# Kernel optimization log

Measured on AMD Instinct MI355X. Metric: run time of the kernel, lower is better.

The kernel has to match this reference:

```python
import jax, jax.numpy as jnp
import numpy as np

B, S, D_IN, D_OUT = 8, 2048, 1024, 64


def setup_inputs() -> dict:
    key = jax.random.key(0)
    ks = jax.random.split(key, 8)
    seq = jax.random.normal(ks[0], (B, S, D_IN), dtype=jnp.float32)
    mask = jax.random.bernoulli(ks[1], 0.15, (B, S))  # True = masked out
    lim = 1.0 / np.sqrt(D_IN)
    Wq = jax.random.uniform(ks[2], (D_IN, D_OUT), jnp.float32, -lim, lim)
    bq = jax.random.uniform(ks[3], (D_OUT,), jnp.float32, -lim, lim)
    Wk = jax.random.uniform(ks[4], (D_IN, D_OUT), jnp.float32, -lim, lim)
    bk = jax.random.uniform(ks[5], (D_OUT,), jnp.float32, -lim, lim)
    Wv = jax.random.uniform(ks[6], (D_IN, D_OUT), jnp.float32, -lim, lim)
    bv = jax.random.uniform(ks[7], (D_OUT,), jnp.float32, -lim, lim)
    return {"seq": seq, "mask": mask, "Wq": Wq, "bq": bq, "Wk": Wk, "bk": bk, "Wv": Wv, "bv": bv}


def reference(seq, mask, Wq, bq, Wk, bk, Wv, bv):
    q = jnp.einsum('bsd,df->bsf', seq, Wq) + bq  # [B,S,D_OUT]
    k = jnp.einsum('bsd,df->bsf', seq, Wk) + bk
    v = jnp.einsum('bsd,df->bsf', seq, Wv) + bv
    # NOTE: original code scales by sqrt(query.shape[1]) == sqrt(S), not sqrt(d)
    scale = jnp.asarray(q.shape[1], q.dtype) ** 0.5
    scores = jnp.einsum('bqf,bkf->bqk', q, k) / scale  # [B,S,S]
    scores = jnp.where(mask[:, None, :], jnp.asarray(-1e9, scores.dtype), scores)
    attn = jax.nn.softmax(scores, axis=-1)
    context = jnp.einsum('bqk,bkf->bqf', attn, v)  # [B,S,D_OUT]
    return context
```

## Files before the change

### kernel.cpp

```cpp
#include <hip/hip_runtime.h>
#include <hip/hip_bf16.h>
#include <stdint.h>

#define NB 8
#define SS 2048
#define DIN 1024
#define DOUT 64
#define MTOT (NB*SS)
#define SCALE 0.02209708691207961f

typedef short  short8 __attribute__((ext_vector_type(8)));
typedef float  f32x4  __attribute__((ext_vector_type(4)));
typedef unsigned short us4 __attribute__((ext_vector_type(4)));

#define WT_OFF 0
#define FM_OFF 393216
#define Q_OFF  524288
#define K_OFF  (Q_OFF + MTOT*DOUT*2)
#define VT_OFF (K_OFF + MTOT*DOUT*2)

__device__ __forceinline__ short f2bf(float f) {
  __bf16 h = (__bf16)f;
  return __builtin_bit_cast(short, h);
}

__device__ __forceinline__ void gl_lds16(const void* g, void* l) {
  __builtin_amdgcn_global_load_lds(
      (const __attribute__((address_space(1))) uint32_t*)g,
      (__attribute__((address_space(3))) uint32_t*)l, 16, 0, 0);
}

__global__ void k_prep(const float* __restrict__ Wq, const float* __restrict__ Wk,
                       const float* __restrict__ Wv, const void* __restrict__ mraw,
                       __bf16* __restrict__ Wt, float* __restrict__ fm) {
  int bid = blockIdx.x, t = threadIdx.x;
  if (bid < 48) {
    __shared__ float tile[64][65];
    int m = bid >> 4;
    int k0 = (bid & 15) * 64;
    const float* W = (m == 0) ? Wq : (m == 1 ? Wk : Wv);
    float sc = (m == 0) ? SCALE : 1.0f;
    #pragma unroll
    for (int i = 0; i < 16; i++) {
      int idx = i*256 + t;
      tile[idx >> 6][idx & 63] = W[(size_t)(k0 + (idx >> 6))*DOUT + (idx & 63)] * sc;
    }
    __syncthreads();
    #pragma unroll
    for (int i = 0; i < 16; i++) {
      int idx = i*256 + t;
      int n = idx >> 6, kk = idx & 63;
      Wt[(size_t)(m*DOUT + n)*DIN + k0 + kk] = (__bf16)tile[kk][n];
    }
  } else {
    __shared__ int bad[2];
    if (t < 2) bad[t] = 0;
    __syncthreads();
    const uint32_t* w = (const uint32_t*)mraw;
    int b0 = 0, b1 = 0;
    for (int i = t; i < 4096; i += 256) {
      uint32_t v = w[i];
      b0 |= !(v == 0u || v == 1u);
      b1 |= !(v == 0u || v == 0x3F800000u);
    }
    if (b0) atomicOr(&bad[0], 1);
    if (b1) atomicOr(&bad[1], 1);
    __syncthreads();
    int u8mode = bad[0] && bad[1];
    const uint8_t* p8 = (const uint8_t*)mraw;
    int i = (bid - 48)*256 + t;
    int mv = u8mode ? (p8[i] != 0) : (w[i] != 0u);
    fm[i] = mv ? 0.0f : 1.0f;
  }
}

__global__ __launch_bounds__(256) void k_qkv(
    const float* __restrict__ seq, const __bf16* __restrict__ Wt,
    const float* __restrict__ bq, const float* __restrict__ bk,
    const float* __restrict__ bv,
    __bf16* __restrict__ Qo, __bf16* __restrict__ Ko, __bf16* __restrict__ Vto) {
  __shared__ uint8_t smem[81920];
  int t = threadIdx.x, w = t >> 6, lane = t & 63, lg = lane >> 4, ll = lane & 15;
  int m0 = blockIdx.x * 64;
  const uint8_t* seqB = (const uint8_t*)seq;
  const uint8_t* WtB  = (const uint8_t*)Wt;

  f32x4 acc[12];
  #pragma unroll
  for (int i = 0; i < 12; i++) acc[i] = f32x4{0.f,0.f,0.f,0.f};

  auto STAGE = [&](int c) {
    uint8_t* bufA = smem + (c & 1)*40960;
    uint8_t* bufB = bufA + 16384;
    #pragma unroll
    for (int j = 0; j < 4; j++) {
      int g = j*256 + w*64 + lane;
      int r = g >> 4, u1 = g & 15;
      int u = u1 ^ (((r & 7) << 1) | ((r >> 3) & 1));
      gl_lds16(seqB + (size_t)(m0 + r)*4096 + c*256 + u*16,
               bufA + (j*256 + w*64)*16);
    }
    #pragma unroll
    for (int j = 0; j < 6; j++) {
      int g = j*256 + w*64 + lane;
      int R = g >> 3, u1 = g & 7;
      int u = u1 ^ (R & 7);
      gl_lds16(WtB + (size_t)R*2048 + c*128 + u*16,
               bufB + (j*256 + w*64)*16);
    }
  };

  STAGE(0);
  __syncthreads();
  for (int c = 0; c < 16; c++) {
    if (c < 15) STAGE(c + 1);
    uint8_t* bufA = smem + (c & 1)*40960;
    uint8_t* bufB = bufA + 16384;
    int r = w*16 + ll;
    int sa = ((r & 7) << 1) | ((r >> 3) & 1);
    short8 ab[2];
    #pragma unroll
    for (int kk = 0; kk < 2; kk++) {
      f32x4 a0 = *(const f32x4*)(bufA + r*256 + (((kk*8 + lg*2    ) ^ sa)*16));
      f32x4 a1 = *(const f32x4*)(bufA + r*256 + (((kk*8 + lg*2 + 1) ^ sa)*16));
      #pragma unroll
      for (int j = 0; j < 4; j++) { ab[kk][j] = f2bf(a0[j]); ab[kk][4+j] = f2bf(a1[j]); }
    }
    #pragma unroll
    for (int kk = 0; kk < 2; kk++) {
      #pragma unroll
      for (int mm = 0; mm < 12; mm++) {
        int R = mm*16 + ll;
        short8 bb = *(const short8*)(bufB + R*128 + (((kk*4 + lg) ^ (R & 7))*16));
        acc[mm] = __builtin_amdgcn_mfma_f32_16x16x32_bf16(ab[kk], bb, acc[mm], 0, 0, 0);
      }
    }
    __syncthreads();
  }

  int orow = m0 + w*16 + lg*4;
  int bb_  = orow >> 11;
  int sloc = orow & 2047;
  #pragma unroll
  for (int mm = 0; mm < 12; mm++) {
    int mat = mm >> 2;
    int col = (mm & 3)*16 + ll;
    float bias = (mat == 0) ? bq[col]*SCALE : (mat == 1 ? bk[col] : bv[col]);
    if (mat == 0) {
      #pragma unroll
      for (int rr = 0; rr < 4; rr++)
        Qo[(size_t)(orow + rr)*DOUT + col] = (__bf16)(acc[mm][rr] + bias);
    } else if (mat == 1) {
      #pragma unroll
      for (int rr = 0; rr < 4; rr++)
        Ko[(size_t)(orow + rr)*DOUT + col] = (__bf16)(acc[mm][rr] + bias);
    } else {
      us4 pk;
      #pragma unroll
      for (int rr = 0; rr < 4; rr++) pk[rr] = (unsigned short)f2bf(acc[mm][rr] + bias);
      *(us4*)((uint8_t*)Vto + ((size_t)(bb_*DOUT + col)*SS + sloc)*2) = pk;
    }
  }
}

__global__ __launch_bounds__(256) void k_attn(
    const __bf16* __restrict__ Q, const __bf16* __restrict__ Kd,
    const __bf16* __restrict__ Vt, const float* __restrict__ fm,
    float* __restrict__ out) {
  __shared__ uint8_t smem[90112];
  float* fml = (float*)(smem + 81920);
  int t = threadIdx.x, w = t >> 6, lane = t & 63, lg = lane >> 4, ll = lane & 15;
  int b = blockIdx.x >> 5, qt = blockIdx.x & 31;
  int q0 = qt*64 + w*16;

  for (int i = t; i < SS; i += 256) fml[i] = fm[b*SS + i];

  const uint8_t* qbase = (const uint8_t*)Q + ((size_t)(b*SS + q0 + ll))*128;
  short8 aq[2];
  aq[0] = *(const short8*)(qbase + lg*16);
  aq[1] = *(const short8*)(qbase + 64 + lg*16);

  f32x4 oacc[4];
  #pragma unroll
  for (int i = 0; i < 4; i++) oacc[i] = f32x4{0.f,0.f,0.f,0.f};
  float den[4] = {0.f, 0.f, 0.f, 0.f};

  const uint8_t* kgb = (const uint8_t*)Kd + (size_t)b*SS*128;
  const uint8_t* vgb = (const uint8_t*)Vt + (size_t)b*DOUT*SS*2;
  uint8_t* pbase = smem + 65536 + w*4096;

  auto STAGE = [&](int kb, int bi) {
    uint8_t* bk_ = smem + bi*32768;
    uint8_t* bv_ = bk_ + 16384;
    #pragma unroll
    for (int j = 0; j < 4; j++) {
      int g = j*256 + w*64 + lane;
      int key = g >> 3, u1 = g & 7;
      int u = u1 ^ (key & 7);
      gl_lds16(kgb + (size_t)(kb*128 + key)*128 + u*16, bk_ + (j*256 + w*64)*16);
    }
    #pragma unroll
    for (int j = 0; j < 4; j++) {
      int g = j*256 + w*64 + lane;
      int d = g >> 4, u1 = g & 15;
      int u = u1 ^ (d & 15);
      gl_lds16(vgb + (size_t)d*4096 + kb*256 + u*16, bv_ + (j*256 + w*64)*16);
    }
  };

  STAGE(0, 0);
  __syncthreads();
  for (int kb = 0; kb < 16; kb++) {
    if (kb < 15) STAGE(kb + 1, (kb + 1) & 1);
    uint8_t* bk_ = smem + (kb & 1)*32768;
    uint8_t* bv_ = bk_ + 16384;
    f32x4 sacc[8];
    #pragma unroll
    for (int i = 0; i < 8; i++) sacc[i] = f32x4{0.f,0.f,0.f,0.f};
    #pragma unroll
    for (int kk = 0; kk < 2; kk++) {
      #pragma unroll
      for (int nf = 0; nf < 8; nf++) {
        int key = nf*16 + ll;
        short8 kf = *(const short8*)(bk_ + key*128 + (((kk*4 + lg) ^ (key & 7))*16));
        sacc[nf] = __builtin_amdgcn_mfma_f32_16x16x32_bf16(aq[kk], kf, sacc[nf], 0, 0, 0);
      }
    }
    #pragma unroll
    for (int nf = 0; nf < 8; nf++) {
      float msk = fml[kb*128 + nf*16 + ll];
      #pragma unroll
      for (int r = 0; r < 4; r++) {
        float p = msk * __expf(sacc[nf][r]);
        __bf16 pb = (__bf16)p;
        den[r] += (float)pb;
        int qrow = lg*4 + r;
        int col = nf*16 + ll;
        *(__bf16*)(pbase + qrow*256 + (((col >> 3) ^ qrow)*16) + (col & 7)*2) = pb;
      }
    }
    #pragma unroll
    for (int ks = 0; ks < 4; ks++) {
      int u = ks*4 + lg;
      short8 pf = *(const short8*)(pbase + ll*256 + ((u ^ ll)*16));
      #pragma unroll
      for (int df = 0; df < 4; df++) {
        int d = df*16 + ll;
        short8 vf = *(const short8*)(bv_ + d*256 + ((u ^ (d & 15))*16));
        oacc[df] = __builtin_amdgcn_mfma_f32_16x16x32_bf16(pf, vf, oacc[df], 0, 0, 0);
      }
    }
    __syncthreads();
  }
  #pragma unroll
  for (int r = 0; r < 4; r++) {
    float d = den[r];
    d += __shfl_xor(d, 1, 64);
    d += __shfl_xor(d, 2, 64);
    d += __shfl_xor(d, 4, 64);
    d += __shfl_xor(d, 8, 64);
    den[r] = d;
  }
  #pragma unroll
  for (int df = 0; df < 4; df++) {
    int col = df*16 + ll;
    #pragma unroll
    for (int r = 0; r < 4; r++) {
      int gq = b*SS + q0 + lg*4 + r;
      out[(size_t)gq*DOUT + col] = oacc[df][r] / den[r];
    }
  }
}

extern "C" void kernel_launch(void* const* d_in, const int* in_sizes, int n_in,
                              void* d_out, int out_size, void* d_ws, size_t ws_size,
                              hipStream_t stream) {
  const float* seq = (const float*)d_in[0];
  const void*  msk = d_in[1];
  const float* Wq  = (const float*)d_in[2];
  const float* bq  = (const float*)d_in[3];
  const float* Wk  = (const float*)d_in[4];
  const float* bk  = (const float*)d_in[5];
  const float* Wv  = (const float*)d_in[6];
  const float* bv  = (const float*)d_in[7];
  uint8_t* ws = (uint8_t*)d_ws;
  __bf16* Wt  = (__bf16*)(ws + WT_OFF);
  float*  fm  = (float*)(ws + FM_OFF);
  __bf16* Qb  = (__bf16*)(ws + Q_OFF);
  __bf16* Kb  = (__bf16*)(ws + K_OFF);
  __bf16* Vtb = (__bf16*)(ws + VT_OFF);
  float* out  = (float*)d_out;

  k_prep<<<dim3(112), dim3(256), 0, stream>>>(Wq, Wk, Wv, msk, Wt, fm);
  k_qkv<<<dim3(256), dim3(256), 0, stream>>>(seq, Wt, bq, bk, bv, Qb, Kb, Vtb);
  k_attn<<<dim3(256), dim3(256), 0, stream>>>(Qb, Kb, Vtb, fm, out);
}
```

Baseline: 147.6 us.

## Triple-buffer LDS staging with explicit vmcnt waits in QKV and attention kernels

Both the QKV projection and attention kernels move from double to triple buffering of the LDS tiles, prefetching two stages ahead. Explicit s_waitcnt vmcnt counts plus a single raw s_barrier per iteration replace the trailing __syncthreads, so global-to-LDS loads can stay in flight across iterations. The aim is to hide more memory latency behind the MFMA work. In exchange, LDS per block grows to 120 KB, which likely cuts resident blocks per CU and may offset the gain.

```diff
diff --git a/kernel.cpp b/kernel.cpp
--- a/kernel.cpp
+++ b/kernel.cpp
@@ -79,7 +79,7 @@
     const float* __restrict__ bq, const float* __restrict__ bk,
     const float* __restrict__ bv,
     __bf16* __restrict__ Qo, __bf16* __restrict__ Ko, __bf16* __restrict__ Vto) {
-  __shared__ uint8_t smem[81920];
+  __shared__ uint8_t smem[122880];
   int t = threadIdx.x, w = t >> 6, lane = t & 63, lg = lane >> 4, ll = lane & 15;
   int m0 = blockIdx.x * 64;
   const uint8_t* seqB = (const uint8_t*)seq;
@@ -89,8 +89,8 @@
   #pragma unroll
   for (int i = 0; i < 12; i++) acc[i] = f32x4{0.f,0.f,0.f,0.f};
 
-  auto STAGE = [&](int c) {
-    uint8_t* bufA = smem + (c & 1)*40960;
+  auto STAGE = [&](int c, int bi) {
+    uint8_t* bufA = smem + bi*40960;
     uint8_t* bufB = bufA + 16384;
     #pragma unroll
     for (int j = 0; j < 4; j++) {
@@ -110,11 +110,17 @@
     }
   };
 
-  STAGE(0);
-  __syncthreads();
+  STAGE(0, 0);
+  STAGE(1, 1);
+  #pragma unroll
   for (int c = 0; c < 16; c++) {
-    if (c < 15) STAGE(c + 1);
-    uint8_t* bufA = smem + (c & 1)*40960;
+    if (c < 15) asm volatile("s_waitcnt vmcnt(10)" ::: "memory");
+    else        asm volatile("s_waitcnt vmcnt(0)"  ::: "memory");
+    __builtin_amdgcn_s_barrier();
+    __builtin_amdgcn_sched_barrier(0);
+    if (c + 2 < 16) STAGE(c + 2, (c + 2) % 3);
+
+    uint8_t* bufA = smem + (c % 3)*40960;
     uint8_t* bufB = bufA + 16384;
     int r = w*16 + ll;
     int sa = ((r & 7) << 1) | ((r >> 3) & 1);
@@ -135,7 +141,6 @@
         acc[mm] = __builtin_amdgcn_mfma_f32_16x16x32_bf16(ab[kk], bb, acc[mm], 0, 0, 0);
       }
     }
-    __syncthreads();
   }
 
   int orow = m0 + w*16 + lg*4;
@@ -167,8 +172,8 @@
     const __bf16* __restrict__ Q, const __bf16* __restrict__ Kd,
     const __bf16* __restrict__ Vt, const float* __restrict__ fm,
     float* __restrict__ out) {
-  __shared__ uint8_t smem[90112];
-  float* fml = (float*)(smem + 81920);
+  __shared__ uint8_t smem[122880];
+  float* fml = (float*)(smem + 114688);
   int t = threadIdx.x, w = t >> 6, lane = t & 63, lg = lane >> 4, ll = lane & 15;
   int b = blockIdx.x >> 5, qt = blockIdx.x & 31;
   int q0 = qt*64 + w*16;
@@ -180,6 +185,8 @@
   aq[0] = *(const short8*)(qbase + lg*16);
   aq[1] = *(const short8*)(qbase + 64 + lg*16);
 
+  asm volatile("s_waitcnt vmcnt(0) lgkmcnt(0)" ::: "memory");
+
   f32x4 oacc[4];
   #pragma unroll
   for (int i = 0; i < 4; i++) oacc[i] = f32x4{0.f,0.f,0.f,0.f};
@@ -187,7 +194,7 @@
 
   const uint8_t* kgb = (const uint8_t*)Kd + (size_t)b*SS*128;
   const uint8_t* vgb = (const uint8_t*)Vt + (size_t)b*DOUT*SS*2;
-  uint8_t* pbase = smem + 65536 + w*4096;
+  uint8_t* pbase = smem + 98304 + w*4096;
 
   auto STAGE = [&](int kb, int bi) {
     uint8_t* bk_ = smem + bi*32768;
@@ -209,10 +216,15 @@
   };
 
   STAGE(0, 0);
-  __syncthreads();
+  STAGE(1, 1);
   for (int kb = 0; kb < 16; kb++) {
-    if (kb < 15) STAGE(kb + 1, (kb + 1) & 1);
-    uint8_t* bk_ = smem + (kb & 1)*32768;
+    if (kb < 15) asm volatile("s_waitcnt vmcnt(8)" ::: "memory");
+    else         asm volatile("s_waitcnt vmcnt(0)" ::: "memory");
+    __builtin_amdgcn_s_barrier();
+    __builtin_amdgcn_sched_barrier(0);
+    if (kb + 2 < 16) STAGE(kb + 2, (kb + 2) % 3);
+
+    uint8_t* bk_ = smem + (kb % 3)*32768;
     uint8_t* bv_ = bk_ + 16384;
     f32x4 sacc[8];
     #pragma unroll
@@ -250,7 +262,6 @@
         oacc[df] = __builtin_amdgcn_mfma_f32_16x16x32_bf16(pf, vf, oacc[df], 0, 0, 0);
       }
     }
-    __syncthreads();
   }
   #pragma unroll
   for (int r = 0; r < 4; r++) {
```

Result: faster. 143.9 us, median of 2 (-2.5%).
